# Kernel optimization log

Measured on AMD Instinct MI355X. Metric: run time of the kernel, lower is better.

Reference implementation:

```python
import jax, jax.numpy as jnp
import numpy as np

N_NODES = 50000
N_EDGES = 800000
IN_SIZE = 256
OUT_SIZE = 256


def setup_inputs() -> dict:
    key = jax.random.key(0)
    k1, k2, k3, k4, k5 = jax.random.split(key, 5)
    x = jax.random.normal(k1, (N_NODES, IN_SIZE), dtype=jnp.float32)
    # nn.Linear default init: U(-1/sqrt(in), 1/sqrt(in)); randn-scaled is fine for a numeric baseline
    bound = 1.0 / np.sqrt(IN_SIZE)
    W = jax.random.uniform(k2, (IN_SIZE, OUT_SIZE), minval=-bound, maxval=bound, dtype=jnp.float32)
    b = jax.random.uniform(k3, (OUT_SIZE,), minval=-bound, maxval=bound, dtype=jnp.float32)
    edge_src = jax.random.randint(k4, (N_EDGES,), 0, N_NODES, dtype=jnp.int32)
    edge_dst = jax.random.randint(k5, (N_EDGES,), 0, N_NODES, dtype=jnp.int32)
    return {"x": x, "W": W, "b": b, "edge_src": edge_src, "edge_dst": edge_dst}


def reference(x, W, b, edge_src, edge_dst):
    # 1) dense projection (nn.Linear):  Wh = x @ W + b   -> [N, out]
    Wh = x @ W + b
    # 2) copy_u: gather source-node projected features per edge -> [E, out]
    m = Wh[edge_src]
    # 3) mean reduce per destination node (DGL fn.mean): zero for isolated nodes
    summed = jax.ops.segment_sum(m, edge_dst, num_segments=N_NODES)  # [N, out]
    deg = jax.ops.segment_sum(jnp.ones((edge_dst.shape[0],), dtype=x.dtype),
                              edge_dst, num_segments=N_NODES)       # [N]
    h = summed / jnp.maximum(deg, 1.0)[:, None]
    return h
```

## Files before the change

kernel.cpp:

```cpp
#include <hip/hip_runtime.h>

#define NN 50000
#define NE 800000
#define DIN 256
#define DOUT 256
#define NSLICE 8
#define QPAD 32
#define ECHUNK 1024
#define NECHUNK ((NE + ECHUNK - 1) / ECHUNK)
#define DRANGE (NN / NSLICE)
#define SLOTS 32
#define OVFCAP 4096

typedef __attribute__((ext_vector_type(8))) short short8;
typedef __attribute__((ext_vector_type(4))) float floatx4;

static __device__ __forceinline__ unsigned short f2bf(float f) {
    unsigned int u = __float_as_uint(f);
    unsigned int r = (u + 0x7fffu + ((u >> 16) & 1u)) >> 16;
    return (unsigned short)r;
}

static __device__ __forceinline__ void gload_lds16(const void* g, void* l) {
    __builtin_amdgcn_global_load_lds(
        (const __attribute__((address_space(1))) unsigned int*)g,
        (__attribute__((address_space(3))) unsigned int*)l, 16, 0, 0);
}

__global__ void zero_ints_kernel(int* __restrict__ p, int n) {
    int i = blockIdx.x * blockDim.x + threadIdx.x;
    if (i < n) p[i] = 0;
}

__global__ __launch_bounds__(256) void prep_kernel(const float* __restrict__ x,
                                                   const float* __restrict__ W,
                                                   unsigned int* __restrict__ xq,
                                                   float* __restrict__ sinv,
                                                   unsigned short* __restrict__ Wt) {
    int bid = blockIdx.x;
    if (bid < 12500) {
        int row = bid * 4 + (threadIdx.x >> 6);
        int lane = threadIdx.x & 63;
        float4 v = *(const float4*)(x + (size_t)row * DIN + lane * 4);
        float m = fmaxf(fmaxf(fabsf(v.x), fabsf(v.y)), fmaxf(fabsf(v.z), fabsf(v.w)));
#pragma unroll
        for (int d = 1; d < 64; d <<= 1) m = fmaxf(m, __shfl_xor(m, d));
        m = fmaxf(m, 1e-20f);
        float sc = 127.0f / m;
        int q0 = (int)rintf(v.x * sc);
        int q1 = (int)rintf(v.y * sc);
        int q2 = (int)rintf(v.z * sc);
        int q3 = (int)rintf(v.w * sc);
        unsigned int pack = (q0 & 255) | ((q1 & 255) << 8) | ((q2 & 255) << 16) | ((q3 & 255) << 24);
        xq[(size_t)row * 64 + lane] = pack;
        if (lane == 0) sinv[row] = m * (1.0f / 127.0f);
    } else {
        int n = bid - 12500;
        int k = threadIdx.x;
        Wt[(size_t)n * DIN + k] = f2bf(W[(size_t)k * DOUT + n]);
    }
}

__global__ __launch_bounds__(256) void scatter_kernel(const int* __restrict__ edge_src,
                                                      const int* __restrict__ edge_dst,
                                                      int* __restrict__ cnt,
                                                      int* __restrict__ qctr,
                                                      int* __restrict__ slots,
                                                      int* __restrict__ ovf_n,
                                                      int* __restrict__ ovf_d,
                                                      int* __restrict__ ovf_s) {
    __shared__ int sh;
    int xcd;
    asm("s_getreg_b32 %0, hwreg(HW_REG_XCC_ID, 0, 32)" : "=s"(xcd));
    xcd &= 7;
    int tid = threadIdx.x;
    if (tid == 0) {
        int found = -1;
        for (int t = 0; t < NSLICE; t++) {
            int q = (xcd + t) & 7;
            int c = atomicAdd(&qctr[q * QPAD], 1);
            if (c < NECHUNK) { found = q * NECHUNK + c; break; }
        }
        sh = found;
    }
    __syncthreads();
    int f = sh;
    if (f < 0) return;
    int q = f / NECHUNK;
    int chunk = f % NECHUNK;
    int dlo = q * DRANGE, dhi = dlo + DRANGE;
    int e0 = chunk * ECHUNK;
#pragma unroll
    for (int k = 0; k < ECHUNK / 256; k++) {
        int e = e0 + k * 256 + tid;
        if (e < NE) {
            int d = __builtin_nontemporal_load(edge_dst + e);
            if (d >= dlo && d < dhi) {
                int src = __builtin_nontemporal_load(edge_src + e);
                int pos = atomicAdd(&cnt[d], 1);
                if (pos < SLOTS) {
                    slots[(d << 5) + pos] = src;
                } else {
                    int oi = atomicAdd(ovf_n, 1);
                    if (oi < OVFCAP) { ovf_d[oi] = d; ovf_s[oi] = src; }
                }
            }
        }
    }
}

__global__ __launch_bounds__(256) void mean_kernel(const unsigned int* __restrict__ xq,
                                                   const float* __restrict__ sinv,
                                                   const int* __restrict__ cnt,
                                                   const int* __restrict__ slots,
                                                   const int* __restrict__ ovf_n,
                                                   const int* __restrict__ ovf_d,
                                                   const int* __restrict__ ovf_s,
                                                   unsigned short* __restrict__ xm) {
    int node = blockIdx.x * 4 + (threadIdx.x >> 6);
    int lane = threadIdx.x & 63;
    int half = lane >> 5;
    int cg = lane & 31;
    int cv = cnt[node];
    int end = (cv < SLOTS) ? cv : SLOTS;
    const int* sp = slots + (node << 5);
    const unsigned int* xcol = xq + cg * 2;
    float a[8];
#pragma unroll
    for (int j = 0; j < 8; j++) a[j] = 0.f;
    int i = half;
    for (; i + 6 < end; i += 8) {
        int s0 = sp[i], s1 = sp[i + 2], s2 = sp[i + 4], s3 = sp[i + 6];
        float c0 = sinv[s0], c1 = sinv[s1], c2 = sinv[s2], c3 = sinv[s3];
        int2 q0 = *(const int2*)(xcol + (size_t)s0 * 64);
        int2 q1 = *(const int2*)(xcol + (size_t)s1 * 64);
        int2 q2 = *(const int2*)(xcol + (size_t)s2 * 64);
        int2 q3 = *(const int2*)(xcol + (size_t)s3 * 64);
#pragma unroll
        for (int j = 0; j < 4; j++) {
            int sh = 8 * j;
            a[j]     += c0 * (float)((signed char)(q0.x >> sh))
                      + c1 * (float)((signed char)(q1.x >> sh))
                      + c2 * (float)((signed char)(q2.x >> sh))
                      + c3 * (float)((signed char)(q3.x >> sh));
            a[4 + j] += c0 * (float)((signed char)(q0.y >> sh))
                      + c1 * (float)((signed char)(q1.y >> sh))
                      + c2 * (float)((signed char)(q2.y >> sh))
                      + c3 * (float)((signed char)(q3.y >> sh));
        }
    }
    for (; i < end; i += 2) {
        int s = sp[i];
        float c = sinv[s];
        int2 qv = *(const int2*)(xcol + (size_t)s * 64);
#pragma unroll
        for (int j = 0; j < 4; j++) {
            int sh = 8 * j;
            a[j]     += c * (float)((signed char)(qv.x >> sh));
            a[4 + j] += c * (float)((signed char)(qv.y >> sh));
        }
    }
    if (cv > SLOTS && half == 0) {
        int n = *ovf_n;
        if (n > OVFCAP) n = OVFCAP;
        for (int k = 0; k < n; k++) {
            if (ovf_d[k] == node) {
                int s = ovf_s[k];
                float c = sinv[s];
                int2 qv = *(const int2*)(xcol + (size_t)s * 64);
#pragma unroll
                for (int j = 0; j < 4; j++) {
                    int sh = 8 * j;
                    a[j]     += c * (float)((signed char)(qv.x >> sh));
                    a[4 + j] += c * (float)((signed char)(qv.y >> sh));
                }
            }
        }
    }
#pragma unroll
    for (int j = 0; j < 8; j++) a[j] += __shfl_xor(a[j], 32);
    float inv = (cv > 0) ? 1.0f / (float)cv : 0.f;
    if (half == 0) {
        short8 o;
#pragma unroll
        for (int j = 0; j < 8; j++) o[j] = (short)f2bf(a[j] * inv);
        *(short8*)(xm + (size_t)node * DIN + cg * 8) = o;
    }
}

__global__ __launch_bounds__(256) void gemm_mfma_kernel(const unsigned short* __restrict__ xm,
                                                        const unsigned short* __restrict__ Wt,
                                                        const float* __restrict__ b,
                                                        const int* __restrict__ cnt,
                                                        float* __restrict__ out) {
    __shared__ unsigned short As[128 * 32];
    __shared__ unsigned short Bs[128 * 32];
    int tid = threadIdx.x;
    int bm = blockIdx.x >> 1;
    int bn = blockIdx.x & 1;
    int row0 = bm * 128, col0 = bn * 128;
    int wave = tid >> 6, lane = tid & 63;
    int wr = wave >> 1, wc = wave & 1;
    int l15 = lane & 15, kgrp = lane >> 4;

    floatx4 acc[4][4];
#pragma unroll
    for (int m = 0; m < 4; m++)
#pragma unroll
        for (int n = 0; n < 4; n++) acc[m][n] = (floatx4){0.f, 0.f, 0.f, 0.f};

    int srow = tid >> 2;
    int kchunk = (tid & 3) * 8;

    for (int kc = 0; kc < DIN; kc += 32) {
#pragma unroll
        for (int i = 0; i < 2; i++) {
            int row = i * 64 + srow;
            int ga_row = row0 + row; if (ga_row >= NN) ga_row = NN - 1;
            gload_lds16(xm + (size_t)ga_row * DIN + kc + kchunk,
                        (char*)As + i * 4096 + wave * 1024);
            gload_lds16(Wt + (size_t)(col0 + row) * DIN + kc + kchunk,
                        (char*)Bs + i * 4096 + wave * 1024);
        }
        __syncthreads();

        short8 af[4], bf[4];
#pragma unroll
        for (int m = 0; m < 4; m++)
            af[m] = *(const short8*)&As[(wr * 64 + m * 16 + l15) * 32 + kgrp * 8];
#pragma unroll
        for (int n = 0; n < 4; n++)
            bf[n] = *(const short8*)&Bs[(wc * 64 + n * 16 + l15) * 32 + kgrp * 8];
#pragma unroll
        for (int m = 0; m < 4; m++)
#pragma unroll
            for (int n = 0; n < 4; n++)
                acc[m][n] = __builtin_amdgcn_mfma_f32_16x16x32_bf16(af[m], bf[n], acc[m][n], 0, 0, 0);
        __syncthreads();
    }

    float bias[4];
#pragma unroll
    for (int n = 0; n < 4; n++) bias[n] = b[col0 + wc * 64 + n * 16 + l15];

#pragma unroll
    for (int m = 0; m < 4; m++) {
#pragma unroll
        for (int r = 0; r < 4; r++) {
            int row = row0 + wr * 64 + m * 16 + kgrp * 4 + r;
            if (row < NN) {
                int dg = cnt[row];
#pragma unroll
                for (int n = 0; n < 4; n++) {
                    int col = col0 + wc * 64 + n * 16 + l15;
                    out[(size_t)row * DOUT + col] = (dg > 0) ? acc[m][n][r] + bias[n] : 0.f;
                }
            }
        }
    }
}

extern "C" void kernel_launch(void* const* d_in, const int* in_sizes, int n_in,
                              void* d_out, int out_size, void* d_ws, size_t ws_size,
                              hipStream_t stream) {
    const float* x = (const float*)d_in[0];
    const float* W = (const float*)d_in[1];
    const float* b = (const float*)d_in[2];
    const int* esrc = (const int*)d_in[3];
    const int* edst = (const int*)d_in[4];
    float* out = (float*)d_out;

    char* ws = (char*)d_ws;
    size_t off = 0;
    unsigned int* xq = (unsigned int*)(ws + off); off += (size_t)NN * DIN;
    unsigned short* xm = (unsigned short*)(ws + off); off += (size_t)NN * DIN * 2;
    float* sinv = (float*)(ws + off); off += (size_t)NN * sizeof(float);
    unsigned short* Wt = (unsigned short*)(ws + off); off += (size_t)DIN * DOUT * 2;
    int* slots = (int*)(ws + off); off += (size_t)NN * SLOTS * sizeof(int);
    int* cnt = (int*)(ws + off); off += (size_t)NN * sizeof(int);
    int* qctrS = (int*)(ws + off); off += (size_t)NSLICE * QPAD * sizeof(int);
    int* ovf_n = (int*)(ws + off); off += 4 * sizeof(int);
    int* ovf_d = (int*)(ws + off); off += OVFCAP * sizeof(int);
    int* ovf_s = (int*)(ws + off); off += OVFCAP * sizeof(int);

    const int nzero = NN + NSLICE * QPAD + 4;
    zero_ints_kernel<<<(nzero + 255) / 256, 256, 0, stream>>>(cnt, nzero);
    prep_kernel<<<12500 + 256, 256, 0, stream>>>(x, W, xq, sinv, Wt);
    scatter_kernel<<<NSLICE * NECHUNK, 256, 0, stream>>>(esrc, edst, cnt, qctrS, slots,
                                                         ovf_n, ovf_d, ovf_s);
    mean_kernel<<<NN / 4, 256, 0, stream>>>(xq, sinv, cnt, slots, ovf_n, ovf_d, ovf_s, xm);
    gemm_mfma_kernel<<<391 * 2, 256, 0, stream>>>(xm, Wt, b, cnt, out);
}
```

Before: 124.3 us.

## Fuse prep and scatter into one kernel and store slot indices as u16

Merges the quantization/transpose prep kernel and the edge scatter kernel into a single launch, so scatter blocks can run alongside the tail of prep instead of waiting on a kernel boundary. Slot source indices are narrowed from 32-bit to 16-bit, which halves the traffic for slot writes and reads; this is valid because node ids fit below 65536. Nontemporal loads on the edge arrays are replaced with ordinary loads. The fused kernel's heavier register footprint now applies to every block.

```diff
diff --git a/kernel.cpp b/kernel.cpp
--- a/kernel.cpp
+++ b/kernel.cpp
@@ -11,6 +11,7 @@
 #define DRANGE (NN / NSLICE)
 #define SLOTS 32
 #define OVFCAP 4096
+#define PREP_BLKS 12756
 
 typedef __attribute__((ext_vector_type(8))) short short8;
 typedef __attribute__((ext_vector_type(4))) float floatx4;
@@ -32,11 +33,19 @@
     if (i < n) p[i] = 0;
 }
 
-__global__ __launch_bounds__(256) void prep_kernel(const float* __restrict__ x,
+__global__ __launch_bounds__(256) void work_kernel(const float* __restrict__ x,
                                                    const float* __restrict__ W,
                                                    unsigned int* __restrict__ xq,
                                                    float* __restrict__ sinv,
-                                                   unsigned short* __restrict__ Wt) {
+                                                   unsigned short* __restrict__ Wt,
+                                                   const int* __restrict__ edge_src,
+                                                   const int* __restrict__ edge_dst,
+                                                   int* __restrict__ cnt,
+                                                   int* __restrict__ qctr,
+                                                   unsigned short* __restrict__ slots,
+                                                   int* __restrict__ ovf_n,
+                                                   int* __restrict__ ovf_d,
+                                                   int* __restrict__ ovf_s) {
     int bid = blockIdx.x;
     if (bid < 12500) {
         int row = bid * 4 + (threadIdx.x >> 6);
@@ -54,21 +63,14 @@
         unsigned int pack = (q0 & 255) | ((q1 & 255) << 8) | ((q2 & 255) << 16) | ((q3 & 255) << 24);
         xq[(size_t)row * 64 + lane] = pack;
         if (lane == 0) sinv[row] = m * (1.0f / 127.0f);
-    } else {
+        return;
+    }
+    if (bid < PREP_BLKS) {
         int n = bid - 12500;
         int k = threadIdx.x;
         Wt[(size_t)n * DIN + k] = f2bf(W[(size_t)k * DOUT + n]);
-    }
-}
-
-__global__ __launch_bounds__(256) void scatter_kernel(const int* __restrict__ edge_src,
-                                                      const int* __restrict__ edge_dst,
-                                                      int* __restrict__ cnt,
-                                                      int* __restrict__ qctr,
-                                                      int* __restrict__ slots,
-                                                      int* __restrict__ ovf_n,
-                                                      int* __restrict__ ovf_d,
-                                                      int* __restrict__ ovf_s) {
+        return;
+    }
     __shared__ int sh;
     int xcd;
     asm("s_getreg_b32 %0, hwreg(HW_REG_XCC_ID, 0, 32)" : "=s"(xcd));
@@ -94,12 +96,12 @@
     for (int k = 0; k < ECHUNK / 256; k++) {
         int e = e0 + k * 256 + tid;
         if (e < NE) {
-            int d = __builtin_nontemporal_load(edge_dst + e);
+            int d = edge_dst[e];
             if (d >= dlo && d < dhi) {
-                int src = __builtin_nontemporal_load(edge_src + e);
+                int src = edge_src[e];
                 int pos = atomicAdd(&cnt[d], 1);
                 if (pos < SLOTS) {
-                    slots[(d << 5) + pos] = src;
+                    slots[(d << 5) + pos] = (unsigned short)src;
                 } else {
                     int oi = atomicAdd(ovf_n, 1);
                     if (oi < OVFCAP) { ovf_d[oi] = d; ovf_s[oi] = src; }
@@ -112,7 +114,7 @@
 __global__ __launch_bounds__(256) void mean_kernel(const unsigned int* __restrict__ xq,
                                                    const float* __restrict__ sinv,
                                                    const int* __restrict__ cnt,
-                                                   const int* __restrict__ slots,
+                                                   const unsigned short* __restrict__ slots,
                                                    const int* __restrict__ ovf_n,
                                                    const int* __restrict__ ovf_d,
                                                    const int* __restrict__ ovf_s,
@@ -123,7 +125,7 @@
     int cg = lane & 31;
     int cv = cnt[node];
     int end = (cv < SLOTS) ? cv : SLOTS;
-    const int* sp = slots + (node << 5);
+    const unsigned short* sp = slots + (node << 5);
     const unsigned int* xcol = xq + cg * 2;
     float a[8];
 #pragma unroll
@@ -276,7 +278,7 @@
     unsigned short* xm = (unsigned short*)(ws + off); off += (size_t)NN * DIN * 2;
     float* sinv = (float*)(ws + off); off += (size_t)NN * sizeof(float);
     unsigned short* Wt = (unsigned short*)(ws + off); off += (size_t)DIN * DOUT * 2;
-    int* slots = (int*)(ws + off); off += (size_t)NN * SLOTS * sizeof(int);
+    unsigned short* slots = (unsigned short*)(ws + off); off += (size_t)NN * SLOTS * 2;
     int* cnt = (int*)(ws + off); off += (size_t)NN * sizeof(int);
     int* qctrS = (int*)(ws + off); off += (size_t)NSLICE * QPAD * sizeof(int);
     int* ovf_n = (int*)(ws + off); off += 4 * sizeof(int);
@@ -285,9 +287,8 @@
 
     const int nzero = NN + NSLICE * QPAD + 4;
     zero_ints_kernel<<<(nzero + 255) / 256, 256, 0, stream>>>(cnt, nzero);
-    prep_kernel<<<12500 + 256, 256, 0, stream>>>(x, W, xq, sinv, Wt);
-    scatter_kernel<<<NSLICE * NECHUNK, 256, 0, stream>>>(esrc, edst, cnt, qctrS, slots,
-                                                         ovf_n, ovf_d, ovf_s);
+    work_kernel<<<PREP_BLKS + NSLICE * NECHUNK, 256, 0, stream>>>(
+        x, W, xq, sinv, Wt, esrc, edst, cnt, qctrS, slots, ovf_n, ovf_d, ovf_s);
     mean_kernel<<<NN / 4, 256, 0, stream>>>(xq, sinv, cnt, slots, ovf_n, ovf_d, ovf_s, xm);
     gemm_mfma_kernel<<<391 * 2, 256, 0, stream>>>(xm, Wt, b, cnt, out);
 }
```

Result: faster. 115.7 us (-6.9%).
